# Kernel tuning notes

Measured on AMD Instinct MI355X. Metric: run time of the kernel, lower is better.

The kernel has to match this reference:

```python
import jax, jax.numpy as jnp
import numpy as np

B, NA, E, H = 256, 128, 1024, 16
HD = E // H  # head_dim = 64
EPS = 1e-5


def _ln(x, w, b):
    m = x.mean(-1, keepdims=True)
    v = x.var(-1, keepdims=True)
    return (x - m) / jnp.sqrt(v + EPS) * w + b


def setup_inputs() -> dict:
    key = jax.random.key(0)
    k0, k1 = jax.random.split(key)
    return {
        "x": jax.random.normal(k0, (B, NA, E), jnp.float32),
        "ln1_w": jnp.ones((E,), jnp.float32),
        "ln1_b": jnp.zeros((E,), jnp.float32),
        # xavier_uniform-ish scale for (3E, E)
        "in_w": jax.random.normal(k1, (3 * E, E), jnp.float32) * (1.0 / np.sqrt(E)),
        "in_b": jnp.zeros((3 * E,), jnp.float32),
        "ln2_w": jnp.ones((E,), jnp.float32),
        "ln2_b": jnp.zeros((E,), jnp.float32),
    }


def reference(x, ln1_w, ln1_b, in_w, in_b, ln2_w, ln2_b):
    bsz, na, e = x.shape
    xn = _ln(x, ln1_w, ln1_b)  # x = ln1(x) in the original (residual uses this)
    qkv = xn @ in_w.T + in_b  # (bsz, na, 3E)
    q, k, v = jnp.split(qkv, 3, axis=-1)
    q = q * (float(HD) ** -0.5)
    # Faithful to torch's contiguous().view(na, bsz*H, HD).transpose(0, 1):
    # a raw row-major reshape of the (bsz, na, E) buffer.
    def _heads(t):
        return t.reshape(na, bsz * H, HD).swapaxes(0, 1)  # (bsz*H, na, HD)
    q, k, v = _heads(q), _heads(k), _heads(v)
    scores = jnp.einsum('bnd,bmd->bnm', q, k)  # (bsz*H, na, na)
    w = jax.nn.softmax(scores, axis=-1)
    attn = jnp.einsum('bnm,bmd->bnd', w, v)  # (bsz*H, na, HD)
    attn = attn.swapaxes(0, 1).reshape(bsz, na, e)
    out = _ln(xn + attn, ln2_w, ln2_b)
    # Faithful quirk: sum over dim=1 (query dim) of (bsz*H, na, na), / num_heads
    avg_w = w.sum(axis=1) / H  # (bsz*H, na)
    return out, avg_w
```

## Files before the change

### kernel.cpp

```cpp
#include <hip/hip_runtime.h>


typedef __attribute__((ext_vector_type(4))) float float4v;
typedef __attribute__((ext_vector_type(4))) int   int4v;
typedef __attribute__((ext_vector_type(8))) short short8v;
typedef __attribute__((ext_vector_type(4))) short short4v;

#define LN_EPS 1e-5f

#define GLL(g, l) __builtin_amdgcn_global_load_lds( \
    (const __attribute__((address_space(1))) unsigned int*)(g), \
    (__attribute__((address_space(3))) unsigned int*)(l), 16, 0, 0)

__device__ __forceinline__ unsigned short f2bf(float f) {
    unsigned int u = __float_as_uint(f);
    u += 0x7FFFu + ((u >> 16) & 1u);
    return (unsigned short)(u >> 16);
}
__device__ __forceinline__ float bf2f(unsigned short h) {
    return __uint_as_float(((unsigned int)h) << 16);
}
__device__ __forceinline__ unsigned int pk_bf16(float lo, float hi) {
    unsigned int r;
    asm("v_cvt_pk_bf16_f32 %0, %1, %2" : "=v"(r) : "v"(lo), "v"(hi));
    return r;
}

__global__ __launch_bounds__(256) void k0_w_to_bf16(const float* __restrict__ w,
                                                    unsigned short* __restrict__ wb) {
    int idx = blockIdx.x * 256 + threadIdx.x;
    const float4v* src = (const float4v*)w;
    float4v a = src[idx * 2];
    float4v b = src[idx * 2 + 1];
    short8v o;
    o[0] = (short)f2bf(a[0]); o[1] = (short)f2bf(a[1]);
    o[2] = (short)f2bf(a[2]); o[3] = (short)f2bf(a[3]);
    o[4] = (short)f2bf(b[0]); o[5] = (short)f2bf(b[1]);
    o[6] = (short)f2bf(b[2]); o[7] = (short)f2bf(b[3]);
    *((short8v*)wb + idx) = o;
}

__global__ __launch_bounds__(256) void k1_ln1(const float* __restrict__ x,
                                              const float* __restrict__ w1,
                                              const float* __restrict__ b1,
                                              unsigned short* __restrict__ xnb) {
    int lane = threadIdx.x & 63;
    int wave = threadIdx.x >> 6;
    int row  = blockIdx.x * 4 + wave;
    const float4v* xr = (const float4v*)(x + (size_t)row * 1024);
    float4v xv[4];
    float s = 0.f, s2 = 0.f;
    #pragma unroll
    for (int c = 0; c < 4; ++c) {
        xv[c] = xr[c * 64 + lane];
        #pragma unroll
        for (int e = 0; e < 4; ++e) { s += xv[c][e]; s2 += xv[c][e] * xv[c][e]; }
    }
    #pragma unroll
    for (int off = 32; off > 0; off >>= 1) {
        s  += __shfl_xor(s, off, 64);
        s2 += __shfl_xor(s2, off, 64);
    }
    float mean = s * (1.0f / 1024.0f);
    float var  = s2 * (1.0f / 1024.0f) - mean * mean;
    float rs   = rsqrtf(var + LN_EPS);
    #pragma unroll
    for (int c = 0; c < 4; ++c) {
        int idx = c * 64 + lane;
        float4v wv = ((const float4v*)w1)[idx];
        float4v bv = ((const float4v*)b1)[idx];
        short4v o;
        #pragma unroll
        for (int e = 0; e < 4; ++e)
            o[e] = (short)f2bf((xv[c][e] - mean) * rs * wv[e] + bv[e]);
        ((short4v*)(xnb + (size_t)row * 1024))[idx] = o;
    }
}

__global__ __launch_bounds__(512, 2) void k2_qkv_gemm(const unsigned short* __restrict__ A,
                                                      const unsigned short* __restrict__ W,
                                                      const float* __restrict__ bias,
                                                      unsigned short* __restrict__ Qb,
                                                      unsigned short* __restrict__ Kb,
                                                      unsigned short* __restrict__ Vb) {
    __shared__ unsigned short smem[65536];
    unsigned short* sA0 = smem;
    unsigned short* sA1 = smem + 16384;
    unsigned short* sB0 = smem + 32768;
    unsigned short* sB1 = smem + 49152;

    int bid = blockIdx.x;
    int wg  = (bid & 7) * 192 + (bid >> 3);
    int nT  = wg % 12;
    int mT  = wg / 12;
    int rowBase = mT * 256;
    int colBase = nT * 256;

    int tid  = threadIdx.x;
    int lane = tid & 63;
    int wave = tid >> 6;
    int wm = wave >> 2, wn = wave & 3;
    int q4 = lane >> 4, l15 = lane & 15;

    int lrow_s = tid >> 3;
    int srcCol = ((tid & 7) * 16) ^ ((lrow_s & 7) << 4);
    const char* aSrc = (const char*)A + ((size_t)(rowBase + lrow_s) << 11) + srcCol;
    const char* wSrc = (const char*)W + ((size_t)(colBase + lrow_s) << 11) + srcCol;
    int waveOff = wave * 1024;

    int xorv = (l15 & 7) << 4;
    int aRow = (wm * 128 + l15) * 128;
    int bRow = (wn * 64 + l15) * 128;
    int bc0 = (q4 * 16) ^ xorv;
    int bc1 = (64 + q4 * 16) ^ xorv;

    float bv[4];
    #pragma unroll
    for (int n = 0; n < 4; ++n) bv[n] = bias[colBase + wn * 64 + n * 16 + l15];

    float4v acc[8][4];
    #pragma unroll
    for (int t = 0; t < 8; ++t)
        #pragma unroll
        for (int n = 0; n < 4; ++n) acc[t][n] = (float4v){0.f, 0.f, 0.f, 0.f};

#define STAGE_HALF(lds, src, ktB_, h) do { \
    GLL((src) + (ktB_) + (2*(h))   * 131072, (char*)(lds) + (2*(h))   * 8192 + waveOff); \
    GLL((src) + (ktB_) + (2*(h)+1) * 131072, (char*)(lds) + (2*(h)+1) * 8192 + waveOff); \
} while (0)
#define LDB(SB) do { \
    const char* c_ = (const char*)(SB); \
    _Pragma("unroll") \
    for (int n = 0; n < 4; ++n) { \
        bf[n][0] = *(const short8v*)(c_ + bRow + n * 2048 + bc0); \
        bf[n][1] = *(const short8v*)(c_ + bRow + n * 2048 + bc1); \
    } \
} while (0)
#define LDA2(SA, T0_) do { \
    const char* c_ = (const char*)(SA); \
    af[0][0] = *(const short8v*)(c_ + aRow + (T0_)     * 2048 + bc0); \
    af[0][1] = *(const short8v*)(c_ + aRow + (T0_)     * 2048 + bc1); \
    af[1][0] = *(const short8v*)(c_ + aRow + (T0_ + 1) * 2048 + bc0); \
    af[1][1] = *(const short8v*)(c_ + aRow + (T0_ + 1) * 2048 + bc1); \
} while (0)
#define MFMA8(T0_) do { \
    __builtin_amdgcn_s_setprio(1); \
    _Pragma("unroll") \
    for (int n = 0; n < 4; ++n) { \
        acc[T0_][n]     = __builtin_amdgcn_mfma_f32_16x16x32_bf16(af[0][0], bf[n][0], acc[T0_][n], 0, 0, 0); \
        acc[T0_][n]     = __builtin_amdgcn_mfma_f32_16x16x32_bf16(af[0][1], bf[n][1], acc[T0_][n], 0, 0, 0); \
        acc[T0_ + 1][n] = __builtin_amdgcn_mfma_f32_16x16x32_bf16(af[1][0], bf[n][0], acc[T0_ + 1][n], 0, 0, 0); \
        acc[T0_ + 1][n] = __builtin_amdgcn_mfma_f32_16x16x32_bf16(af[1][1], bf[n][1], acc[T0_ + 1][n], 0, 0, 0); \
    } \
    __builtin_amdgcn_s_setprio(0); \
} while (0)
#define PH_SYNC do { __builtin_amdgcn_s_barrier(); asm volatile("s_waitcnt lgkmcnt(0)"); } while (0)
#define PH_END  __builtin_amdgcn_s_barrier()

    STAGE_HALF(sA0, aSrc, 0, 0);
    STAGE_HALF(sA0, aSrc, 0, 1);
    STAGE_HALF(sB0, wSrc, 0, 0);
    STAGE_HALF(sB0, wSrc, 0, 1);
    STAGE_HALF(sB1, wSrc, 128, 0);
    STAGE_HALF(sB1, wSrc, 128, 1);
    asm volatile("s_waitcnt vmcnt(4)");
    __builtin_amdgcn_s_barrier();

    short8v af[2][2], bf[4][2];

    #pragma unroll 1
    for (int i = 0; i < 8; ++i) {
        int ktB = i << 8;
        bool nl = (i < 7);
        LDB(sB0); LDA2(sA0, 0);
        STAGE_HALF(sA1, aSrc, ktB + 128, 0);
        PH_SYNC; MFMA8(0); PH_END;
        LDA2(sA0, 2);
        STAGE_HALF(sA1, aSrc, ktB + 128, 1);
        PH_SYNC; MFMA8(2); PH_END;
        LDA2(sA0, 4);
        if (nl) STAGE_HALF(sB0, wSrc, ktB + 256, 0);
        PH_SYNC; MFMA8(4); PH_END;
        LDA2(sA0, 6);
        if (nl) { STAGE_HALF(sB0, wSrc, ktB + 256, 1); asm volatile("s_waitcnt vmcnt(4)"); }
        else    { asm volatile("s_waitcnt vmcnt(0)"); }
        PH_SYNC; MFMA8(6); PH_END;
        LDB(sB1); LDA2(sA1, 0);
        if (nl) STAGE_HALF(sA0, aSrc, ktB + 256, 0);
        PH_SYNC; MFMA8(0); PH_END;
        LDA2(sA1, 2);
        if (nl) STAGE_HALF(sA0, aSrc, ktB + 256, 1);
        PH_SYNC; MFMA8(2); PH_END;
        LDA2(sA1, 4);
        if (nl) STAGE_HALF(sB1, wSrc, ktB + 384, 0);
        PH_SYNC; MFMA8(4); PH_END;
        LDA2(sA1, 6);
        if (nl) { STAGE_HALF(sB1, wSrc, ktB + 384, 1); asm volatile("s_waitcnt vmcnt(4)"); }
        PH_SYNC; MFMA8(6); PH_END;
    }
#undef STAGE_HALF
#undef LDB
#undef LDA2
#undef MFMA8
#undef PH_SYNC
#undef PH_END

    __syncthreads();
    float scale = (colBase < 1024) ? 0.125f : 1.0f;
    unsigned short* outb = (colBase < 1024) ? Qb : (colBase < 2048) ? Kb : Vb;
    int lcol = colBase & 1023;
    #pragma unroll
    for (int t = 0; t < 8; ++t)
        #pragma unroll
        for (int n = 0; n < 4; ++n)
            #pragma unroll
            for (int g = 0; g < 4; ++g) {
                int row  = wm * 128 + t * 16 + q4 * 4 + g;
                int colb = (wn * 64 + n * 16 + l15) * 2;
                *(unsigned short*)((char*)smem + row * 512 + (colb ^ ((row & 7) << 4))) =
                    f2bf((acc[t][n][g] + bv[n]) * scale);
            }
    __syncthreads();
    #pragma unroll
    for (int k = 0; k < 16; ++k) {
        int r = k * 16 + (tid >> 5);
        short8v v = *(const short8v*)((const char*)smem + r * 512 + (tid & 31) * 16);
        int colb = ((tid & 31) * 16) ^ ((r & 7) << 4);
        *(short8v*)((char*)(outb + (size_t)(rowBase + r) * 1024 + lcol) + colb) = v;
    }
}

__global__ __launch_bounds__(256) void k2b_vtrans(const unsigned short* __restrict__ Vb,
                                                  unsigned short* __restrict__ Vt) {
    int g  = blockIdx.x * 256 + threadIdx.x;
    int ib = g & 15;
    int db = (g >> 4) & 7;
    int j  = g >> 7;
    const unsigned short* src = Vb + (size_t)(ib * 8) * 262144 + (size_t)j * 64 + db * 8;
    short8v in[8];
    #pragma unroll
    for (int r = 0; r < 8; ++r)
        in[r] = *(const short8v*)(src + (size_t)r * 262144);
    unsigned short* dst = Vt + (size_t)j * 8192 + (db * 8) * 128 + ib * 8;
    #pragma unroll
    for (int c = 0; c < 8; ++c) {
        short8v o;
        #pragma unroll
        for (int r = 0; r < 8; ++r) o[r] = in[r][c];
        *(short8v*)(dst + c * 128) = o;
    }
}

__global__ __launch_bounds__(256) void k3_attn(const unsigned short* __restrict__ Qb,
                                               const unsigned short* __restrict__ Kb,
                                               const unsigned short* __restrict__ Vt,
                                               unsigned short* __restrict__ attnb,
                                               float* __restrict__ avgw) {
    __shared__ unsigned short smem[34816];
    __shared__ float csum[2][2][128];

    int tid = threadIdx.x;
    int lane = tid & 63;
    int wave = tid >> 6;
    int grp = wave >> 1, wm = wave & 1;
    int j = blockIdx.x * 2 + grp;
    int q4 = lane >> 4, l15 = lane & 15;

    unsigned short* sQ = smem + grp * 8192;
    unsigned short* sK = smem + 16384 + grp * 8192;
    char* sP = (char*)smem + wave * 17408;

    csum[0][tid >> 7][tid & 127] = 0.f;
    csum[1][tid >> 7][tid & 127] = 0.f;

    {
        const char* qg = (const char*)(Qb + (size_t)j * 64);
        const char* kg = (const char*)(Kb + (size_t)j * 64);
        int swz = ((lane & 7) ^ (lane >> 3)) << 4;
        #pragma unroll
        for (int blk = 0; blk < 8; ++blk) {
            int row0 = wm * 64 + blk * 8;
            size_t src = (size_t)(row0 + (lane >> 3)) * 524288 + swz;
            GLL(qg + src, (char*)sQ + row0 * 128);
            GLL(kg + src, (char*)sK + row0 * 128);
        }
    }
    __syncthreads();

    float4v S[8][4];
    #pragma unroll
    for (int a = 0; a < 8; ++a)
        #pragma unroll
        for (int b = 0; b < 4; ++b) S[a][b] = (float4v){0.f, 0.f, 0.f, 0.f};
    #pragma unroll
    for (int ks = 0; ks < 2; ++ks) {
        int cb = (ks * 64 + q4 * 16) ^ ((l15 & 7) << 4);
        short8v qf[4];
        #pragma unroll
        for (int tm = 0; tm < 4; ++tm)
            qf[tm] = *(const short8v*)((const char*)sQ + (wm * 64 + tm * 16 + l15) * 128 + cb);
        #pragma unroll
        for (int tn = 0; tn < 8; ++tn) {
            short8v kf = *(const short8v*)((const char*)sK + (tn * 16 + l15) * 128 + cb);
            #pragma unroll
            for (int tm = 0; tm < 4; ++tm)
                S[tn][tm] = __builtin_amdgcn_mfma_f32_16x16x32_bf16(kf, qf[tm], S[tn][tm], 0, 0, 0);
        }
    }
    __syncthreads();

    const char* vg = (const char*)Vt + (size_t)j * 16384;
    short8v vf0[4], vf1[4];
    #pragma unroll
    for (int t = 0; t < 4; ++t)
        vf0[t] = *(const short8v*)(vg + (t * 16 + l15) * 256 + q4 * 16);

    float rmax[4], inv[4];
    #pragma unroll
    for (int tm = 0; tm < 4; ++tm) {
        float m0 = S[0][tm][0];
        #pragma unroll
        for (int tn = 0; tn < 8; ++tn)
            #pragma unroll
            for (int g = 0; g < 4; ++g) m0 = fmaxf(m0, S[tn][tm][g]);
        m0 = fmaxf(m0, __shfl_xor(m0, 16, 64));
        m0 = fmaxf(m0, __shfl_xor(m0, 32, 64));
        rmax[tm] = m0;
    }
    #pragma unroll
    for (int tm = 0; tm < 4; ++tm) {
        float t0 = 0.f;
        #pragma unroll
        for (int tn = 0; tn < 8; ++tn)
            #pragma unroll
            for (int g = 0; g < 4; ++g) {
                float e = __expf(S[tn][tm][g] - rmax[tm]);
                S[tn][tm][g] = e;
                t0 += e;
            }
        t0 += __shfl_xor(t0, 16, 64);
        t0 += __shfl_xor(t0, 32, 64);
        inv[tm] = 1.0f / t0;
    }
    #pragma unroll
    for (int tn = 0; tn < 8; ++tn)
        #pragma unroll
        for (int tm = 0; tm < 4; ++tm)
            #pragma unroll
            for (int g = 0; g < 4; ++g) S[tn][tm][g] *= inv[tm];

    #pragma unroll
    for (int tn = 0; tn < 8; ++tn) {
        #pragma unroll
        for (int g = 0; g < 4; ++g) {
            float cs = S[tn][0][g] + S[tn][1][g] + S[tn][2][g] + S[tn][3][g];
            cs += __shfl_xor(cs, 1, 64);
            cs += __shfl_xor(cs, 2, 64);
            cs += __shfl_xor(cs, 4, 64);
            cs += __shfl_xor(cs, 8, 64);
            if (l15 == 0) csum[wm][grp][tn * 16 + q4 * 4 + g] = cs;
        }
    }

    #pragma unroll
    for (int tn = 0; tn < 8; ++tn)
        #pragma unroll
        for (int tm = 0; tm < 4; ++tm)
            #pragma unroll
            for (int p = 0; p < 2; ++p) {
                unsigned int pk = pk_bf16(S[tn][tm][2 * p], S[tn][tm][2 * p + 1]);
                *(unsigned int*)(sP + (tm * 16 + l15) * 272 +
                                 (tn * 16 + q4 * 4 + 2 * p) * 2) = pk;
            }

    float4v O[4][4];
    #pragma unroll
    for (int a = 0; a < 4; ++a)
        #pragma unroll
        for (int b = 0; b < 4; ++b) O[a][b] = (float4v){0.f, 0.f, 0.f, 0.f};
    #pragma unroll
    for (int ks = 0; ks < 4; ++ks) {
        if (ks < 3) {
            #pragma unroll
            for (int t = 0; t < 4; ++t)
                vf1[t] = *(const short8v*)(vg + (t * 16 + l15) * 256 + (ks + 1) * 64 + q4 * 16);
        }
        short8v pf[4];
        #pragma unroll
        for (int tm = 0; tm < 4; ++tm)
            pf[tm] = *(const short8v*)(sP + (tm * 16 + l15) * 272 + ks * 64 + q4 * 16);
        #pragma unroll
        for (int tm = 0; tm < 4; ++tm)
            #pragma unroll
            for (int tno = 0; tno < 4; ++tno)
                O[tm][tno] = __builtin_amdgcn_mfma_f32_16x16x32_bf16(pf[tm], vf0[tno], O[tm][tno], 0, 0, 0);
        #pragma unroll
        for (int t = 0; t < 4; ++t) vf0[t] = vf1[t];
    }

    size_t base = (size_t)j * 64;
    #pragma unroll
    for (int tm = 0; tm < 4; ++tm)
        #pragma unroll
        for (int tno = 0; tno < 4; ++tno)
            #pragma unroll
            for (int g = 0; g < 4; ++g) {
                int m = wm * 64 + tm * 16 + q4 * 4 + g;
                int d = tno * 16 + l15;
                attnb[base + (size_t)m * 262144 + d] = f2bf(O[tm][tno][g]);
            }

    __syncthreads();
    {
        int g2 = tid >> 7, n = tid & 127;
        avgw[(size_t)(blockIdx.x * 2 + g2) * 128 + n] =
            (csum[0][g2][n] + csum[1][g2][n]) * (1.0f / 16.0f);
    }
}

__global__ __launch_bounds__(256) void k4_ln2(const float* __restrict__ x,
                                              const float* __restrict__ w1,
                                              const float* __restrict__ b1,
                                              const unsigned short* __restrict__ attnb,
                                              const float* __restrict__ w2,
                                              const float* __restrict__ b2,
                                              float* __restrict__ out) {
    int lane = threadIdx.x & 63;
    int wave = threadIdx.x >> 6;
    int row  = blockIdx.x * 4 + wave;
    const float4v* xr = (const float4v*)(x + (size_t)row * 1024);
    float4v xv[4];
    float s = 0.f, s2 = 0.f;
    #pragma unroll
    for (int c = 0; c < 4; ++c) {
        xv[c] = xr[c * 64 + lane];
        #pragma unroll
        for (int e = 0; e < 4; ++e) { s += xv[c][e]; s2 += xv[c][e] * xv[c][e]; }
    }
    #pragma unroll
    for (int off = 32; off > 0; off >>= 1) {
        s  += __shfl_xor(s, off, 64);
        s2 += __shfl_xor(s2, off, 64);
    }
    float mean = s * (1.0f / 1024.0f);
    float var  = s2 * (1.0f / 1024.0f) - mean * mean;
    float rs   = rsqrtf(var + LN_EPS);
    float4v r[4];
    s = 0.f; s2 = 0.f;
    #pragma unroll
    for (int c = 0; c < 4; ++c) {
        int idx = c * 64 + lane;
        float4v wv = ((const float4v*)w1)[idx];
        float4v bv = ((const float4v*)b1)[idx];
        short4v av = ((const short4v*)(attnb + (size_t)row * 1024))[idx];
        #pragma unroll
        for (int e = 0; e < 4; ++e) {
            r[c][e] = (xv[c][e] - mean) * rs * wv[e] + bv[e] + bf2f((unsigned short)av[e]);
            s += r[c][e]; s2 += r[c][e] * r[c][e];
        }
    }
    #pragma unroll
    for (int off = 32; off > 0; off >>= 1) {
        s  += __shfl_xor(s, off, 64);
        s2 += __shfl_xor(s2, off, 64);
    }
    float mean2 = s * (1.0f / 1024.0f);
    float var2  = s2 * (1.0f / 1024.0f) - mean2 * mean2;
    float rs2   = rsqrtf(var2 + LN_EPS);
    #pragma unroll
    for (int c = 0; c < 4; ++c) {
        int idx = c * 64 + lane;
        float4v w2v = ((const float4v*)w2)[idx];
        float4v b2v = ((const float4v*)b2)[idx];
        float4v o;
        #pragma unroll
        for (int e = 0; e < 4; ++e)
            o[e] = (r[c][e] - mean2) * rs2 * w2v[e] + b2v[e];
        ((float4v*)(out + (size_t)row * 1024))[idx] = o;
    }
}

extern "C" void kernel_launch(void* const* d_in, const int* in_sizes, int n_in,
                              void* d_out, int out_size, void* d_ws, size_t ws_size,
                              hipStream_t stream) {
    const float* x    = (const float*)d_in[0];
    const float* ln1w = (const float*)d_in[1];
    const float* ln1b = (const float*)d_in[2];
    const float* inw  = (const float*)d_in[3];
    const float* inb  = (const float*)d_in[4];
    const float* ln2w = (const float*)d_in[5];
    const float* ln2b = (const float*)d_in[6];
    float* out  = (float*)d_out;
    float* avgw = out + 33554432;

    char* ws = (char*)d_ws;
    unsigned short* xnb   = (unsigned short*)(ws);
    unsigned short* Vt    = (unsigned short*)(ws);
    unsigned short* Qb    = (unsigned short*)(ws + 67108864);
    unsigned short* Kb    = (unsigned short*)(ws + 134217728);
    unsigned short* Vb    = (unsigned short*)(ws + 201326592);
    unsigned short* attnb = (unsigned short*)(ws + 201326592);
    unsigned short* Wb    = (unsigned short*)(ws + 268435456);

    k0_w_to_bf16<<<1536, 256, 0, stream>>>(inw, Wb);
    k1_ln1<<<8192, 256, 0, stream>>>(x, ln1w, ln1b, xnb);
    k2_qkv_gemm<<<1536, 512, 0, stream>>>(xnb, Wb, inb, Qb, Kb, Vb);
    k2b_vtrans<<<2048, 256, 0, stream>>>(Vb, Vt);
    k3_attn<<<2048, 256, 0, stream>>>(Qb, Kb, Vt, attnb, avgw);
    k4_ln2<<<8192, 256, 0, stream>>>(x, ln1w, ln1b, attnb, ln2w, ln2b, out);
}
```

Measured before the change: 632.3 us.

## Write QKV in per-head contiguous layout and fuse V transpose into attention

The GEMM now gathers A rows in a permuted order so each output tile maps to whole heads. It writes Q/K/V as contiguous 128x64 per-head blocks instead of strided rows. The separate V-transpose kernel is removed: attention loads V contiguously and transposes it into shared memory, with one head per 128-thread block. This removes a kernel launch and a full V round trip, and makes attention loads contiguous. In exchange the GEMM's A-loads become scattered rows and the attention output stores change pattern.

```diff
diff --git a/kernel.cpp b/kernel.cpp
--- a/kernel.cpp
+++ b/kernel.cpp
@@ -80,9 +80,9 @@
 __global__ __launch_bounds__(512, 2) void k2_qkv_gemm(const unsigned short* __restrict__ A,
                                                       const unsigned short* __restrict__ W,
                                                       const float* __restrict__ bias,
-                                                      unsigned short* __restrict__ Qb,
-                                                      unsigned short* __restrict__ Kb,
-                                                      unsigned short* __restrict__ Vb) {
+                                                      unsigned short* __restrict__ Qg,
+                                                      unsigned short* __restrict__ Kg,
+                                                      unsigned short* __restrict__ Vg) {
     __shared__ unsigned short smem[65536];
     unsigned short* sA0 = smem;
     unsigned short* sA1 = smem + 16384;
@@ -93,7 +93,6 @@
     int wg  = (bid & 7) * 192 + (bid >> 3);
     int nT  = wg % 12;
     int mT  = wg / 12;
-    int rowBase = mT * 256;
     int colBase = nT * 256;
 
     int tid  = threadIdx.x;
@@ -104,7 +103,13 @@
 
     int lrow_s = tid >> 3;
     int srcCol = ((tid & 7) * 16) ^ ((lrow_s & 7) << 4);
-    const char* aSrc = (const char*)A + ((size_t)(rowBase + lrow_s) << 11) + srcCol;
+    const char* aQ[4];
+    #pragma unroll
+    for (int q = 0; q < 4; ++q) {
+        int trow = q * 64 + lrow_s;
+        size_t m = (size_t)(trow & 127) * 256 + (size_t)(mT * 2 + (trow >> 7));
+        aQ[q] = (const char*)A + (m << 11) + srcCol;
+    }
     const char* wSrc = (const char*)W + ((size_t)(colBase + lrow_s) << 11) + srcCol;
     int waveOff = wave * 1024;
 
@@ -124,9 +129,13 @@
         #pragma unroll
         for (int n = 0; n < 4; ++n) acc[t][n] = (float4v){0.f, 0.f, 0.f, 0.f};
 
-#define STAGE_HALF(lds, src, ktB_, h) do { \
-    GLL((src) + (ktB_) + (2*(h))   * 131072, (char*)(lds) + (2*(h))   * 8192 + waveOff); \
-    GLL((src) + (ktB_) + (2*(h)+1) * 131072, (char*)(lds) + (2*(h)+1) * 8192 + waveOff); \
+#define STAGE_A(lds, ktB_, h) do { \
+    GLL(aQ[2*(h)]   + (ktB_), (char*)(lds) + (2*(h))   * 8192 + waveOff); \
+    GLL(aQ[2*(h)+1] + (ktB_), (char*)(lds) + (2*(h)+1) * 8192 + waveOff); \
+} while (0)
+#define STAGE_W(lds, ktB_, h) do { \
+    GLL(wSrc + (ktB_) + (2*(h))   * 131072, (char*)(lds) + (2*(h))   * 8192 + waveOff); \
+    GLL(wSrc + (ktB_) + (2*(h)+1) * 131072, (char*)(lds) + (2*(h)+1) * 8192 + waveOff); \
 } while (0)
 #define LDB(SB) do { \
     const char* c_ = (const char*)(SB); \
@@ -157,12 +166,12 @@
 #define PH_SYNC do { __builtin_amdgcn_s_barrier(); asm volatile("s_waitcnt lgkmcnt(0)"); } while (0)
 #define PH_END  __builtin_amdgcn_s_barrier()
 
-    STAGE_HALF(sA0, aSrc, 0, 0);
-    STAGE_HALF(sA0, aSrc, 0, 1);
-    STAGE_HALF(sB0, wSrc, 0, 0);
-    STAGE_HALF(sB0, wSrc, 0, 1);
-    STAGE_HALF(sB1, wSrc, 128, 0);
-    STAGE_HALF(sB1, wSrc, 128, 1);
+    STAGE_A(sA0, 0, 0);
+    STAGE_A(sA0, 0, 1);
+    STAGE_W(sB0, 0, 0);
+    STAGE_W(sB0, 0, 1);
+    STAGE_W(sB1, 128, 0);
+    STAGE_W(sB1, 128, 1);
     asm volatile("s_waitcnt vmcnt(4)");
     __builtin_amdgcn_s_barrier();
 
@@ -173,32 +182,33 @@
         int ktB = i << 8;
         bool nl = (i < 7);
         LDB(sB0); LDA2(sA0, 0);
-        STAGE_HALF(sA1, aSrc, ktB + 128, 0);
+        STAGE_A(sA1, ktB + 128, 0);
         PH_SYNC; MFMA8(0); PH_END;
         LDA2(sA0, 2);
-        STAGE_HALF(sA1, aSrc, ktB + 128, 1);
+        STAGE_A(sA1, ktB + 128, 1);
         PH_SYNC; MFMA8(2); PH_END;
         LDA2(sA0, 4);
-        if (nl) STAGE_HALF(sB0, wSrc, ktB + 256, 0);
+        if (nl) STAGE_W(sB0, ktB + 256, 0);
         PH_SYNC; MFMA8(4); PH_END;
         LDA2(sA0, 6);
-        if (nl) { STAGE_HALF(sB0, wSrc, ktB + 256, 1); asm volatile("s_waitcnt vmcnt(4)"); }
+        if (nl) { STAGE_W(sB0, ktB + 256, 1); asm volatile("s_waitcnt vmcnt(4)"); }
         else    { asm volatile("s_waitcnt vmcnt(0)"); }
         PH_SYNC; MFMA8(6); PH_END;
         LDB(sB1); LDA2(sA1, 0);
-        if (nl) STAGE_HALF(sA0, aSrc, ktB + 256, 0);
+        if (nl) STAGE_A(sA0, ktB + 256, 0);
         PH_SYNC; MFMA8(0); PH_END;
         LDA2(sA1, 2);
-        if (nl) STAGE_HALF(sA0, aSrc, ktB + 256, 1);
+        if (nl) STAGE_A(sA0, ktB + 256, 1);
         PH_SYNC; MFMA8(2); PH_END;
         LDA2(sA1, 4);
-        if (nl) STAGE_HALF(sB1, wSrc, ktB + 384, 0);
+        if (nl) STAGE_W(sB1, ktB + 384, 0);
         PH_SYNC; MFMA8(4); PH_END;
         LDA2(sA1, 6);
-        if (nl) { STAGE_HALF(sB1, wSrc, ktB + 384, 1); asm volatile("s_waitcnt vmcnt(4)"); }
+        if (nl) { STAGE_W(sB1, ktB + 384, 1); asm volatile("s_waitcnt vmcnt(4)"); }
         PH_SYNC; MFMA8(6); PH_END;
     }
-#undef STAGE_HALF
+#undef STAGE_A
+#undef STAGE_W
 #undef LDB
 #undef LDA2
 #undef MFMA8
@@ -207,8 +217,7 @@
 
     __syncthreads();
     float scale = (colBase < 1024) ? 0.125f : 1.0f;
-    unsigned short* outb = (colBase < 1024) ? Qb : (colBase < 2048) ? Kb : Vb;
-    int lcol = colBase & 1023;
+    unsigned short* outb = (colBase < 1024) ? Qg : (colBase < 2048) ? Kg : Vg;
     #pragma unroll
     for (int t = 0; t < 8; ++t)
         #pragma unroll
@@ -221,68 +230,60 @@
                     f2bf((acc[t][n][g] + bv[n]) * scale);
             }
     __syncthreads();
-    #pragma unroll
-    for (int k = 0; k < 16; ++k) {
-        int r = k * 16 + (tid >> 5);
-        short8v v = *(const short8v*)((const char*)smem + r * 512 + (tid & 31) * 16);
-        int colb = ((tid & 31) * 16) ^ ((r & 7) << 4);
-        *(short8v*)((char*)(outb + (size_t)(rowBase + r) * 1024 + lcol) + colb) = v;
-    }
-}
-
-__global__ __launch_bounds__(256) void k2b_vtrans(const unsigned short* __restrict__ Vb,
-                                                  unsigned short* __restrict__ Vt) {
-    int g  = blockIdx.x * 256 + threadIdx.x;
-    int ib = g & 15;
-    int db = (g >> 4) & 7;
-    int j  = g >> 7;
-    const unsigned short* src = Vb + (size_t)(ib * 8) * 262144 + (size_t)j * 64 + db * 8;
-    short8v in[8];
-    #pragma unroll
-    for (int r = 0; r < 8; ++r)
-        in[r] = *(const short8v*)(src + (size_t)r * 262144);
-    unsigned short* dst = Vt + (size_t)j * 8192 + (db * 8) * 128 + ib * 8;
-    #pragma unroll
-    for (int c = 0; c < 8; ++c) {
-        short8v o;
-        #pragma unroll
-        for (int r = 0; r < 8; ++r) o[r] = in[r][c];
-        *(short8v*)(dst + c * 128) = o;
-    }
-}
-
-__global__ __launch_bounds__(256) void k3_attn(const unsigned short* __restrict__ Qb,
-                                               const unsigned short* __restrict__ Kb,
-                                               const unsigned short* __restrict__ Vt,
+    {
+        int rr = wave >> 2, c = wave & 3;
+        int jg = (mT * 2 + rr) * 16 + ((colBase & 1023) >> 6) + c;
+        unsigned short* dstG = outb + (size_t)jg * 8192 + (lane & 7) * 8;
+        #pragma unroll
+        for (int it = 0; it < 16; ++it) {
+            int i_na = it * 8 + (lane >> 3);
+            int r = rr * 128 + i_na;
+            int colb = (c * 128 + (lane & 7) * 16) ^ ((r & 7) << 4);
+            short8v v = *(const short8v*)((const char*)smem + r * 512 + colb);
+            *(short8v*)(dstG + (size_t)i_na * 64) = v;
+        }
+    }
+}
+
+__global__ __launch_bounds__(128) void k3_attn(const unsigned short* __restrict__ Qg,
+                                               const unsigned short* __restrict__ Kg,
+                                               const unsigned short* __restrict__ Vg,
                                                unsigned short* __restrict__ attnb,
                                                float* __restrict__ avgw) {
-    __shared__ unsigned short smem[34816];
-    __shared__ float csum[2][2][128];
-
+    __shared__ __attribute__((aligned(128))) char smem[51200];
+    float* csum = (float*)(smem + 50176);
+
+    int j = blockIdx.x;
     int tid = threadIdx.x;
     int lane = tid & 63;
-    int wave = tid >> 6;
-    int grp = wave >> 1, wm = wave & 1;
-    int j = blockIdx.x * 2 + grp;
+    int wm = tid >> 6;
     int q4 = lane >> 4, l15 = lane & 15;
 
-    unsigned short* sQ = smem + grp * 8192;
-    unsigned short* sK = smem + 16384 + grp * 8192;
-    char* sP = (char*)smem + wave * 17408;
-
-    csum[0][tid >> 7][tid & 127] = 0.f;
-    csum[1][tid >> 7][tid & 127] = 0.f;
-
     {
-        const char* qg = (const char*)(Qb + (size_t)j * 64);
-        const char* kg = (const char*)(Kb + (size_t)j * 64);
+        const char* qg = (const char*)(Qg + (size_t)j * 8192);
+        const char* kg = (const char*)(Kg + (size_t)j * 8192);
         int swz = ((lane & 7) ^ (lane >> 3)) << 4;
         #pragma unroll
         for (int blk = 0; blk < 8; ++blk) {
             int row0 = wm * 64 + blk * 8;
-            size_t src = (size_t)(row0 + (lane >> 3)) * 524288 + swz;
-            GLL(qg + src, (char*)sQ + row0 * 128);
-            GLL(kg + src, (char*)sK + row0 * 128);
+            int src = (row0 + (lane >> 3)) * 128 + swz;
+            GLL(qg + src, smem + row0 * 128);
+            GLL(kg + src, smem + 16384 + row0 * 128);
+        }
+    }
+    {
+        int nb = tid & 15, db = tid >> 4;
+        const unsigned short* vsrc = Vg + (size_t)j * 8192 + (nb * 8) * 64 + db * 8;
+        short8v in[8];
+        #pragma unroll
+        for (int k = 0; k < 8; ++k) in[k] = *(const short8v*)(vsrc + k * 64);
+        char* vt = smem + 32768;
+        #pragma unroll
+        for (int c = 0; c < 8; ++c) {
+            short8v o;
+            #pragma unroll
+            for (int k = 0; k < 8; ++k) o[k] = in[k][c];
+            *(short8v*)(vt + (db * 8 + c) * 272 + nb * 16) = o;
         }
     }
     __syncthreads();
@@ -298,22 +299,15 @@
         short8v qf[4];
         #pragma unroll
         for (int tm = 0; tm < 4; ++tm)
-            qf[tm] = *(const short8v*)((const char*)sQ + (wm * 64 + tm * 16 + l15) * 128 + cb);
+            qf[tm] = *(const short8v*)(smem + (wm * 64 + tm * 16 + l15) * 128 + cb);
         #pragma unroll
         for (int tn = 0; tn < 8; ++tn) {
-            short8v kf = *(const short8v*)((const char*)sK + (tn * 16 + l15) * 128 + cb);
+            short8v kf = *(const short8v*)(smem + 16384 + (tn * 16 + l15) * 128 + cb);
             #pragma unroll
             for (int tm = 0; tm < 4; ++tm)
                 S[tn][tm] = __builtin_amdgcn_mfma_f32_16x16x32_bf16(kf, qf[tm], S[tn][tm], 0, 0, 0);
         }
     }
-    __syncthreads();
-
-    const char* vg = (const char*)Vt + (size_t)j * 16384;
-    short8v vf0[4], vf1[4];
-    #pragma unroll
-    for (int t = 0; t < 4; ++t)
-        vf0[t] = *(const short8v*)(vg + (t * 16 + l15) * 256 + q4 * 16);
 
     float rmax[4], inv[4];
     #pragma unroll
@@ -358,64 +352,68 @@
             cs += __shfl_xor(cs, 2, 64);
             cs += __shfl_xor(cs, 4, 64);
             cs += __shfl_xor(cs, 8, 64);
-            if (l15 == 0) csum[wm][grp][tn * 16 + q4 * 4 + g] = cs;
-        }
-    }
-
+            if (l15 == 0) csum[wm * 128 + tn * 16 + q4 * 4 + g] = cs;
+        }
+    }
+    __syncthreads();
+
+    char* sP = smem;
     #pragma unroll
     for (int tn = 0; tn < 8; ++tn)
         #pragma unroll
-        for (int tm = 0; tm < 4; ++tm)
+        for (int tm = 0; tm < 4; ++tm) {
+            int row = wm * 64 + tm * 16 + l15;
+            int swz = (row & 7) << 4;
             #pragma unroll
             for (int p = 0; p < 2; ++p) {
                 unsigned int pk = pk_bf16(S[tn][tm][2 * p], S[tn][tm][2 * p + 1]);
-                *(unsigned int*)(sP + (tm * 16 + l15) * 272 +
-                                 (tn * 16 + q4 * 4 + 2 * p) * 2) = pk;
+                int x = ((tn * 16 + q4 * 4 + 2 * p) * 2) ^ swz;
+                *(unsigned int*)(sP + row * 256 + x) = pk;
             }
+        }
 
     float4v O[4][4];
     #pragma unroll
     for (int a = 0; a < 4; ++a)
         #pragma unroll
         for (int b = 0; b < 4; ++b) O[a][b] = (float4v){0.f, 0.f, 0.f, 0.f};
+    const char* vt = smem + 32768;
     #pragma unroll
     for (int ks = 0; ks < 4; ++ks) {
-        if (ks < 3) {
-            #pragma unroll
-            for (int t = 0; t < 4; ++t)
-                vf1[t] = *(const short8v*)(vg + (t * 16 + l15) * 256 + (ks + 1) * 64 + q4 * 16);
-        }
-        short8v pf[4];
+        int nB = (ks * 32 + q4 * 8) * 2;
+        short8v pf[4], vf[4];
+        #pragma unroll
+        for (int t = 0; t < 4; ++t)
+            vf[t] = *(const short8v*)(vt + (t * 16 + l15) * 272 + nB);
+        #pragma unroll
+        for (int tm = 0; tm < 4; ++tm) {
+            int row = wm * 64 + tm * 16 + l15;
+            pf[tm] = *(const short8v*)(sP + row * 256 + (nB ^ ((row & 7) << 4)));
+        }
         #pragma unroll
         for (int tm = 0; tm < 4; ++tm)
-            pf[tm] = *(const short8v*)(sP + (tm * 16 + l15) * 272 + ks * 64 + q4 * 16);
+            #pragma unroll
+            for (int tno = 0; tno < 4; ++tno)
+                O[tm][tno] = __builtin_amdgcn_mfma_f32_16x16x32_bf16(pf[tm], vf[tno], O[tm][tno], 0, 0, 0);
+    }
+
+    {
+        int jq = j >> 4;
+        int eb = (j & 15) * 64;
         #pragma unroll
         for (int tm = 0; tm < 4; ++tm)
             #pragma unroll
-            for (int tno = 0; tno < 4; ++tno)
-                O[tm][tno] = __builtin_amdgcn_mfma_f32_16x16x32_bf16(pf[tm], vf0[tno], O[tm][tno], 0, 0, 0);
-        #pragma unroll
-        for (int t = 0; t < 4; ++t) vf0[t] = vf1[t];
-    }
-
-    size_t base = (size_t)j * 64;
-    #pragma unroll
-    for (int tm = 0; tm < 4; ++tm)
-        #pragma unroll
-        for (int tno = 0; tno < 4; ++tno)
-            #pragma unroll
             for (int g = 0; g < 4; ++g) {
-                int m = wm * 64 + tm * 16 + q4 * 4 + g;
-                int d = tno * 16 + l15;
-                attnb[base + (size_t)m * 262144 + d] = f2bf(O[tm][tno][g]);
+                int i_na = wm * 64 + tm * 16 + q4 * 4 + g;
+                size_t mrow = (size_t)i_na * 256 + jq;
+                #pragma unroll
+                for (int tno = 0; tno < 4; ++tno)
+                    attnb[mrow * 1024 + eb + tno * 16 + l15] = f2bf(O[tm][tno][g]);
             }
+    }
 
     __syncthreads();
-    {
-        int g2 = tid >> 7, n = tid & 127;
-        avgw[(size_t)(blockIdx.x * 2 + g2) * 128 + n] =
-            (csum[0][g2][n] + csum[1][g2][n]) * (1.0f / 16.0f);
-    }
+    avgw[(size_t)j * 128 + tid] = (csum[tid] + csum[128 + tid]) * (1.0f / 16.0f);
 }
 
 __global__ __launch_bounds__(256) void k4_ln2(const float* __restrict__ x,
@@ -495,17 +493,15 @@
 
     char* ws = (char*)d_ws;
     unsigned short* xnb   = (unsigned short*)(ws);
-    unsigned short* Vt    = (unsigned short*)(ws);
-    unsigned short* Qb    = (unsigned short*)(ws + 67108864);
-    unsigned short* Kb    = (unsigned short*)(ws + 134217728);
-    unsigned short* Vb    = (unsigned short*)(ws + 201326592);
-    unsigned short* attnb = (unsigned short*)(ws + 201326592);
+    unsigned short* attnb = (unsigned short*)(ws);
+    unsigned short* Qg    = (unsigned short*)(ws + 67108864);
+    unsigned short* Kg    = (unsigned short*)(ws + 134217728);
+    unsigned short* Vg    = (unsigned short*)(ws + 201326592);
     unsigned short* Wb    = (unsigned short*)(ws + 268435456);
 
     k0_w_to_bf16<<<1536, 256, 0, stream>>>(inw, Wb);
     k1_ln1<<<8192, 256, 0, stream>>>(x, ln1w, ln1b, xnb);
-    k2_qkv_gemm<<<1536, 512, 0, stream>>>(xnb, Wb, inb, Qb, Kb, Vb);
-    k2b_vtrans<<<2048, 256, 0, stream>>>(Vb, Vt);
-    k3_attn<<<2048, 256, 0, stream>>>(Qb, Kb, Vt, attnb, avgw);
+    k2_qkv_gemm<<<1536, 512, 0, stream>>>(xnb, Wb, inb, Qg, Kg, Vg);
+    k3_attn<<<4096, 128, 0, stream>>>(Qg, Kg, Vg, attnb, avgw);
     k4_ln2<<<8192, 256, 0, stream>>>(x, ln1w, ln1b, attnb, ln2w, ln2b, out);
 }
```

Result: faster. 601.8 us (-4.8%).
